# Kernel optimization log

Hardware: AMD Instinct MI355X
Metric: run time of the kernel (lower is better)

## Reference

```python
import jax, jax.numpy as jnp
import numpy as np

B, S, D = 32, 64, 16
OUT_F = 8
IN_DIM = S * D                      # 1024
N_QUAD = (IN_DIM + IN_DIM ** 2) // 2  # 524800 upper-triangular (incl. diag) entries
OUT_DIM = OUT_F * S                 # 512

# Static upper-triangular indices (row-major, includes diagonal) — same order as
# torch.triu_indices(in_dim, in_dim).
_TRIU_R, _TRIU_C = np.triu_indices(IN_DIM)


def setup_inputs() -> dict:
    key = jax.random.key(0)
    k1, k2, k3 = jax.random.split(key, 3)
    input_ = jax.random.normal(k1, (B, S, D), dtype=jnp.float32)
    in_total = IN_DIM + N_QUAD
    bound = 1.0 / np.sqrt(in_total)
    W = jax.random.uniform(k2, (OUT_DIM, in_total), dtype=jnp.float32, minval=-bound, maxval=bound)
    b = jax.random.uniform(k3, (OUT_DIM,), dtype=jnp.float32, minval=-bound, maxval=bound)
    return {"input_": input_, "W": W, "b": b}


def reference(input_, W, b):
    Bsz = input_.shape[0]
    x_flat = input_.reshape(Bsz, IN_DIM)                     # [B, in_dim]
    r = jnp.asarray(_TRIU_R)
    c = jnp.asarray(_TRIU_C)
    # Quadratic features: upper-triangular entries of outer(x, x) without
    # materializing the full [B, in_dim, in_dim] outer product.
    x_squared = x_flat[:, r] * x_flat[:, c]                  # [B, N_QUAD]
    x = jnp.concatenate([x_flat, x_squared], axis=-1)        # [B, in_dim + N_QUAD]
    out = x @ W.T + b                                        # [B, out_f * S]
    return out.reshape(Bsz, S, OUT_F)
```

## Files before the change

### kernel.cpp

```cpp
#include <hip/hip_runtime.h>
#include <hip/hip_bf16.h>

#define B_SZ     32
#define IN_DIM   1024
#define K_TOTAL  525824
#define OUT_DIM  512
#define NCH      4108
#define KS       64
#define NEED_WS  ((size_t)NCH * 512 * 16)

typedef __attribute__((ext_vector_type(8))) short bfrag;
typedef __attribute__((ext_vector_type(4))) float f32x4;

#define GLD16(g, l) __builtin_amdgcn_global_load_lds(                      \
    (const __attribute__((address_space(1))) void*)(g),                    \
    (__attribute__((address_space(3))) void*)(l), 16, 0, 0)

__device__ inline unsigned bf16r(float f)
{
    unsigned u = __builtin_bit_cast(unsigned, f);
    return (u + 0x7FFFu + ((u >> 16) & 1u)) >> 16;
}
__device__ inline unsigned pk2(float a, float b)
{
    return bf16r(a) | (bf16r(b) << 16);
}

__global__ void bias_init_kernel(const float* __restrict__ bias, float* __restrict__ out)
{
    int i = blockIdx.x * 256 + threadIdx.x;
    out[i] = bias[i & (OUT_DIM - 1)];
}

__global__ __launch_bounds__(256)
void feat_pack_kernel(const float* __restrict__ x, int4* __restrict__ fp)
{
    const int chunk = blockIdx.x;
    const int tid   = threadIdx.x;

    #pragma unroll
    for (int i = 0; i < 2; ++i) {
        const int unit = tid + i * 256;
        const int kb   = unit >> 5;
        const int b    = unit & 31;
        const int k0   = chunk * 128 + kb * 8;
        const float* xb = x + b * IN_DIM;

        float v[8];
        if (chunk < 8) {
            #pragma unroll
            for (int e = 0; e < 8; ++e) v[e] = xb[k0 + e];
        } else {
            int t = k0 - IN_DIM;
            double disc = 4198401.0 - 8.0 * (double)t;
            int r = (int)((2049.0 - sqrt(disc)) * 0.5);
            int off = r * IN_DIM - ((r * (r - 1)) >> 1);
            if (t < off) { --r; off = r * IN_DIM - ((r * (r - 1)) >> 1); }
            else if (t >= off + (IN_DIM - r)) { off += IN_DIM - r; ++r; }
            int c_ = r + (t - off);
            #pragma unroll
            for (int e = 0; e < 8; ++e) {
                v[e] = xb[r] * xb[c_];
                if (c_ == IN_DIM - 1) { ++r; c_ = r; } else { ++c_; }
            }
        }
        int4 pk;
        pk.x = (int)pk2(v[0], v[1]);
        pk.y = (int)pk2(v[2], v[3]);
        pk.z = (int)pk2(v[4], v[5]);
        pk.w = (int)pk2(v[6], v[7]);
        fp[(size_t)chunk * 512 + unit] = pk;
    }
}

__global__ __launch_bounds__(256, 2)
void qgemm_mfma_kernel(const int4* __restrict__ fp,
                       const float* __restrict__ W,
                       float* __restrict__ out)
{
    __shared__ int4 fbuf[3][512];

    const int tid  = threadIdx.x;
    const int lane = tid & 63;
    const int wv_  = tid >> 6;
    const int lrow = lane & 15;
    const int lkb  = lane >> 4;

    const int og = blockIdx.x >> 6;
    const int kg = blockIdx.x & 63;

    const int o_base = og * 64 + wv_ * 16;
    const float* wlane = W + (size_t)(o_base + lrow) * K_TOTAL;
    const char*  fpB   = (const char*)fp + (size_t)lane * 16;

    f32x4 acc0 = {0.f, 0.f, 0.f, 0.f};
    f32x4 acc1 = {0.f, 0.f, 0.f, 0.f};
    float4 wc[8], wn[8];

    #define WLOADR(dst, cc)                                                     \
    do {                                                                        \
        const float* wp_ = wlane + (size_t)(cc) * 128 + lkb * 8;                \
        _Pragma("unroll")                                                       \
        for (int q_ = 0; q_ < 4; ++q_) {                                        \
            dst[2*q_]   = *(const float4*)(wp_ + q_ * 32);                      \
            dst[2*q_+1] = *(const float4*)(wp_ + q_ * 32 + 4);                  \
        }                                                                       \
    } while (0)

    #define STAGEF(s, cc)                                                       \
    do {                                                                        \
        const char* gp_ = fpB + (size_t)(cc) * 8192;                            \
        GLD16(gp_ + wv_ * 1024,        (char*)&fbuf[s][0] + wv_ * 1024);        \
        GLD16(gp_ + 4096 + wv_ * 1024, (char*)&fbuf[s][0] + 4096 + wv_ * 1024); \
    } while (0)

    #define COMPUTE(cbuf)                                                       \
    do {                                                                        \
        const int4* bp_ = &fbuf[cbuf][0];                                       \
        _Pragma("unroll")                                                       \
        for (int q_ = 0; q_ < 4; ++q_) {                                        \
            int4 tw_;                                                           \
            tw_.x = (int)pk2(wc[2*q_].x,   wc[2*q_].y);                         \
            tw_.y = (int)pk2(wc[2*q_].z,   wc[2*q_].w);                         \
            tw_.z = (int)pk2(wc[2*q_+1].x, wc[2*q_+1].y);                       \
            tw_.w = (int)pk2(wc[2*q_+1].z, wc[2*q_+1].w);                       \
            const bfrag bw_ = __builtin_bit_cast(bfrag, tw_);                   \
            const int ub_ = (q_ * 4 + lkb) * 32 + lrow;                         \
            const bfrag a0_ = __builtin_bit_cast(bfrag, bp_[ub_]);              \
            const bfrag a1_ = __builtin_bit_cast(bfrag, bp_[ub_ + 16]);         \
            acc0 = __builtin_amdgcn_mfma_f32_16x16x32_bf16(a0_, bw_, acc0, 0, 0, 0); \
            acc1 = __builtin_amdgcn_mfma_f32_16x16x32_bf16(a1_, bw_, acc1, 0, 0, 0); \
        }                                                                       \
    } while (0)

    int c = kg;
    STAGEF(0, c);
    WLOADR(wn, c);
    STAGEF(1, c + KS);

    int cb = 0, sb = 2;
    for (; c < NCH; c += KS) {
        asm volatile("s_waitcnt vmcnt(2)" ::: "memory");
        __builtin_amdgcn_s_barrier();
        #pragma unroll
        for (int j = 0; j < 8; ++j) wc[j] = wn[j];
        const int cw = (c + KS     < NCH) ? c + KS     : c;
        const int cf = (c + 2 * KS < NCH) ? c + 2 * KS : c;
        WLOADR(wn, cw);
        STAGEF(sb, cf);
        COMPUTE(cb);
        cb = (cb == 2) ? 0 : cb + 1;
        sb = (sb == 2) ? 0 : sb + 1;
    }
    asm volatile("s_waitcnt vmcnt(0)" ::: "memory");

    #undef COMPUTE
    #undef STAGEF
    #undef WLOADR

    float* ob = out + o_base + lrow;
    const int r0 = lkb * 4;
    #pragma unroll
    for (int r = 0; r < 4; ++r) {
        atomicAdd(ob + (size_t)(r0 + r) * OUT_DIM,      acc0[r]);
        atomicAdd(ob + (size_t)(16 + r0 + r) * OUT_DIM, acc1[r]);
    }
}

__global__ __launch_bounds__(512, 2)
void qgemm_fallback_kernel(const float* __restrict__ x,
                           const float* __restrict__ W,
                           float* __restrict__ out)
{
    __shared__ float xt[B_SZ][512];

    const int tid  = threadIdx.x;
    const int lane = tid & 63;
    const int wave = tid >> 6;
    const int bgrp = wave & 3;
    const int ogrp = wave >> 2;

    const int og  = blockIdx.x & 31;
    const int kgf = blockIdx.x >> 5;

    const int o_base = og * 16 + ogrp * 8;
    const int b_base = bgrp * 8;

    float acc[8][8];
    #pragma unroll
    for (int i = 0; i < 8; ++i)
        #pragma unroll
        for (int o = 0; o < 8; ++o) acc[i][o] = 0.f;

    const int nch = (K_TOTAL + 511) / 512;
    for (int chunk = kgf; chunk < nch; chunk += 16) {
        const int k = chunk * 512 + tid;
        __syncthreads();
        if (k < IN_DIM) {
            #pragma unroll
            for (int b = 0; b < B_SZ; ++b)
                xt[b][tid] = x[b * IN_DIM + k];
        } else {
            const int t = k - IN_DIM;
            double disc = 4198401.0 - 8.0 * (double)t;
            int r = (int)((2049.0 - sqrt(disc)) * 0.5);
            int off = r * IN_DIM - ((r * (r - 1)) >> 1);
            if (t < off) { --r; off = r * IN_DIM - ((r * (r - 1)) >> 1); }
            else if (t >= off + (IN_DIM - r)) { off += IN_DIM - r; ++r; }
            const int ccol = r + (t - off);
            #pragma unroll
            for (int b = 0; b < B_SZ; ++b)
                xt[b][tid] = x[b * IN_DIM + r] * x[b * IN_DIM + ccol];
        }
        __syncthreads();

        const float* wrow = W + (size_t)o_base * K_TOTAL + (size_t)chunk * 512;
        #pragma unroll
        for (int pass = 0; pass < 2; ++pass) {
            const int kk = pass * 256 + lane * 4;
            float4 wv[8];
            #pragma unroll
            for (int o = 0; o < 8; ++o)
                wv[o] = *(const float4*)(wrow + (size_t)o * K_TOTAL + kk);
            float4 xv[8];
            #pragma unroll
            for (int i = 0; i < 8; ++i)
                xv[i] = *(const float4*)&xt[b_base + i][kk];
            #pragma unroll
            for (int o = 0; o < 8; ++o)
                #pragma unroll
                for (int i = 0; i < 8; ++i)
                    acc[i][o] += xv[i].x * wv[o].x + xv[i].y * wv[o].y
                               + xv[i].z * wv[o].z + xv[i].w * wv[o].w;
        }
    }

    #pragma unroll
    for (int i = 0; i < 8; ++i)
        #pragma unroll
        for (int o = 0; o < 8; ++o) {
            float v = acc[i][o];
            #pragma unroll
            for (int m = 1; m < 64; m <<= 1)
                v += __shfl_xor(v, m);
            acc[i][o] = v;
        }

    if (lane == 0) {
        #pragma unroll
        for (int i = 0; i < 8; ++i)
            #pragma unroll
            for (int o = 0; o < 8; ++o)
                atomicAdd(&out[(b_base + i) * OUT_DIM + o_base + o], acc[i][o]);
    }
}

extern "C" void kernel_launch(void* const* d_in, const int* in_sizes, int n_in,
                              void* d_out, int out_size, void* d_ws, size_t ws_size,
                              hipStream_t stream)
{
    const float* x    = (const float*)d_in[0];
    const float* W    = (const float*)d_in[1];
    const float* bias = (const float*)d_in[2];
    float* out = (float*)d_out;

    hipLaunchKernelGGL(bias_init_kernel, dim3(64), dim3(256), 0, stream, bias, out);

    if (ws_size >= NEED_WS) {
        int4* fpk = (int4*)d_ws;
        hipLaunchKernelGGL(feat_pack_kernel, dim3(NCH), dim3(256), 0, stream, x, fpk);
        hipLaunchKernelGGL(qgemm_mfma_kernel, dim3(8 * KS), dim3(256), 0, stream,
                           fpk, W, out);
    } else {
        hipLaunchKernelGGL(qgemm_fallback_kernel, dim3(512), dim3(512), 0, stream,
                           x, W, out);
    }
}
```

Measured before the change: 309.3 us.

## Double split-K blocks, replace atomics with partial buffer plus reduce kernel

Raises the split-K factor from 64 to 128 groups, doubling the grid to 1024 blocks, and raises the launch-bounds occupancy hint to 4 blocks per CU. It replaces the atomicAdd epilogue with plain stores into a per-split partial buffer, followed by a separate reduce kernel that adds the bias. It also switches the triangular-index sqrt from double to float. The aim is more parallelism to hide the W streaming, with no atomic contention. The cost is an extra kernel launch, 8MB of partial-sum traffic, and a larger workspace requirement that could push execution onto the fallback path.

```diff
diff --git a/kernel.cpp b/kernel.cpp
--- a/kernel.cpp
+++ b/kernel.cpp
@@ -6,8 +6,10 @@
 #define K_TOTAL  525824
 #define OUT_DIM  512
 #define NCH      4108
-#define KS       64
-#define NEED_WS  ((size_t)NCH * 512 * 16)
+#define KGN      128
+#define F_BYTES  ((size_t)NCH * 8192)
+#define P_ELEMS  ((size_t)KGN * B_SZ * OUT_DIM)
+#define NEED_WS  (F_BYTES + P_ELEMS * 4)
 
 typedef __attribute__((ext_vector_type(8))) short bfrag;
 typedef __attribute__((ext_vector_type(4))) float f32x4;
@@ -52,8 +54,8 @@
             for (int e = 0; e < 8; ++e) v[e] = xb[k0 + e];
         } else {
             int t = k0 - IN_DIM;
-            double disc = 4198401.0 - 8.0 * (double)t;
-            int r = (int)((2049.0 - sqrt(disc)) * 0.5);
+            float disc = 4198401.0f - 8.0f * (float)t;
+            int r = (int)((2049.0f - sqrtf(disc)) * 0.5f);
             int off = r * IN_DIM - ((r * (r - 1)) >> 1);
             if (t < off) { --r; off = r * IN_DIM - ((r * (r - 1)) >> 1); }
             else if (t >= off + (IN_DIM - r)) { off += IN_DIM - r; ++r; }
@@ -73,10 +75,10 @@
     }
 }
 
-__global__ __launch_bounds__(256, 2)
+__global__ __launch_bounds__(256, 4)
 void qgemm_mfma_kernel(const int4* __restrict__ fp,
                        const float* __restrict__ W,
-                       float* __restrict__ out)
+                       float* __restrict__ partial)
 {
     __shared__ int4 fbuf[3][512];
 
@@ -86,8 +88,8 @@
     const int lrow = lane & 15;
     const int lkb  = lane >> 4;
 
-    const int og = blockIdx.x >> 6;
-    const int kg = blockIdx.x & 63;
+    const int og = blockIdx.x >> 7;
+    const int kg = blockIdx.x & (KGN - 1);
 
     const int o_base = og * 64 + wv_ * 16;
     const float* wlane = W + (size_t)(o_base + lrow) * K_TOTAL;
@@ -136,16 +138,16 @@
     int c = kg;
     STAGEF(0, c);
     WLOADR(wn, c);
-    STAGEF(1, c + KS);
+    STAGEF(1, c + KGN);
 
     int cb = 0, sb = 2;
-    for (; c < NCH; c += KS) {
+    for (; c < NCH; c += KGN) {
         asm volatile("s_waitcnt vmcnt(2)" ::: "memory");
         __builtin_amdgcn_s_barrier();
         #pragma unroll
         for (int j = 0; j < 8; ++j) wc[j] = wn[j];
-        const int cw = (c + KS     < NCH) ? c + KS     : c;
-        const int cf = (c + 2 * KS < NCH) ? c + 2 * KS : c;
+        const int cw = (c + KGN     < NCH) ? c + KGN     : c;
+        const int cf = (c + 2 * KGN < NCH) ? c + 2 * KGN : c;
         WLOADR(wn, cw);
         STAGEF(sb, cf);
         COMPUTE(cb);
@@ -158,13 +160,27 @@
     #undef STAGEF
     #undef WLOADR
 
-    float* ob = out + o_base + lrow;
+    float* pb = partial + (size_t)kg * (B_SZ * OUT_DIM) + o_base + lrow;
     const int r0 = lkb * 4;
     #pragma unroll
     for (int r = 0; r < 4; ++r) {
-        atomicAdd(ob + (size_t)(r0 + r) * OUT_DIM,      acc0[r]);
-        atomicAdd(ob + (size_t)(16 + r0 + r) * OUT_DIM, acc1[r]);
-    }
+        pb[(size_t)(r0 + r) * OUT_DIM]      = acc0[r];
+        pb[(size_t)(16 + r0 + r) * OUT_DIM] = acc1[r];
+    }
+}
+
+__global__ __launch_bounds__(256)
+void reduce_kernel(const float* __restrict__ partial,
+                   const float* __restrict__ bias,
+                   float* __restrict__ out)
+{
+    const int idx = blockIdx.x * 256 + threadIdx.x;
+    float s = bias[idx & (OUT_DIM - 1)];
+    const float* p = partial + idx;
+    #pragma unroll 8
+    for (int kg = 0; kg < KGN; ++kg)
+        s += p[(size_t)kg * (B_SZ * OUT_DIM)];
+    out[idx] = s;
 }
 
 __global__ __launch_bounds__(512, 2)
@@ -264,14 +280,16 @@
     const float* bias = (const float*)d_in[2];
     float* out = (float*)d_out;
 
-    hipLaunchKernelGGL(bias_init_kernel, dim3(64), dim3(256), 0, stream, bias, out);
-
     if (ws_size >= NEED_WS) {
-        int4* fpk = (int4*)d_ws;
+        int4*  fpk  = (int4*)d_ws;
+        float* part = (float*)((char*)d_ws + F_BYTES);
         hipLaunchKernelGGL(feat_pack_kernel, dim3(NCH), dim3(256), 0, stream, x, fpk);
-        hipLaunchKernelGGL(qgemm_mfma_kernel, dim3(8 * KS), dim3(256), 0, stream,
-                           fpk, W, out);
+        hipLaunchKernelGGL(qgemm_mfma_kernel, dim3(8 * KGN), dim3(256), 0, stream,
+                           fpk, W, part);
+        hipLaunchKernelGGL(reduce_kernel, dim3(64), dim3(256), 0, stream,
+                           part, bias, out);
     } else {
+        hipLaunchKernelGGL(bias_init_kernel, dim3(64), dim3(256), 0, stream, bias, out);
         hipLaunchKernelGGL(qgemm_fallback_kernel, dim3(512), dim3(512), 0, stream,
                            x, W, out);
     }
```

New measurement: 313.0 us. About the same (+1.2%).
